# Performance work log

Hardware: AMD Instinct MI355X
Metric: run time of the kernel (lower is better)

## Reference

```python
import jax, jax.numpy as jnp
import numpy as np

DROPOUT_P = 0.5  # used as an additive constant in the normalizers, not as dropout
N = 384


def setup_inputs() -> dict:
    key = jax.random.key(0)
    k1, k2 = jax.random.split(key)
    inp = jax.random.uniform(k1, (N, N, N), dtype=jnp.float32)
    w = jax.random.uniform(k2, (N, N, N), dtype=jnp.float32)
    return {"input": inp, "w": w}


def reference(input, w):
    # e[i,j,l] = sum_k input[i,j,k] * w[l,k,j]
    e = jnp.einsum('ijk,lkj->ijl', input, w)
    # k (normalized by input row-sums) is dead code in the original forward;
    # only q and v feed the output, so we skip it.
    v = e  # second identical einsum in the source
    s_in = input.sum(axis=-1, keepdims=True)          # [N, N, 1]
    # einsum('ijk,ijl->ijl', input, w) == (sum_k input) * w
    q = s_in * w
    q = q / (DROPOUT_P + w.sum(axis=-1, keepdims=True))
    # causal mask: strict upper triangle set to -inf, broadcast over batch
    mask = jnp.triu(jnp.full((N, N), -jnp.inf, dtype=q.dtype), k=1)  # [N, N]
    attn = jax.nn.softmax(q + mask[None, :, :], axis=-1)              # [N, N, N]
    return jnp.matmul(attn, v)
```

## Files before the change

### kernel.cpp

```cpp
#include <hip/hip_runtime.h>
#include <hip/hip_bf16.h>


#define N 384
#define N2 (N * N)
#define BK 64
static const size_t N3 = (size_t)N * N * N;

typedef __attribute__((ext_vector_type(8))) short s16x8;
typedef __attribute__((ext_vector_type(4))) float f32x4;

#define AS1 __attribute__((address_space(1)))
#define AS3 __attribute__((address_space(3)))
__device__ __forceinline__ void gll16(const void* g, void* l) {
    __builtin_amdgcn_global_load_lds((const AS1 unsigned int*)g,
                                     (AS3 unsigned int*)l, 16, 0, 0);
}

__device__ __forceinline__ unsigned short f32_to_bf16(float f) {
    unsigned int u = __float_as_uint(f);
    u += 0x7FFFu + ((u >> 16) & 1u);
    return (unsigned short)(u >> 16);
}
__device__ __forceinline__ unsigned int pk2(float a, float b) {
    return (unsigned int)f32_to_bf16(a) | ((unsigned int)f32_to_bf16(b) << 16);
}

__global__ __launch_bounds__(256) void kT(const float* __restrict__ w,
                                          unsigned short* __restrict__ wt) {
    __shared__ unsigned short tile[64][68];
    const int r0 = blockIdx.x * 64;
    const int j0 = blockIdx.y * 64;
    const int tx = threadIdx.x & 63;
    const int ty = threadIdx.x >> 6;
#pragma unroll
    for (int p = 0; p < 16; ++p) {
        const int r = ty * 16 + p;
        tile[r][tx] = f32_to_bf16(w[(size_t)(r0 + r) * N + j0 + tx]);
    }
    __syncthreads();
#pragma unroll
    for (int p = 0; p < 16; ++p) {
        const int jj = ty * 16 + p;
        wt[(size_t)(j0 + jj) * N2 + r0 + tx] = tile[tx][jj];
    }
}

__global__ __launch_bounds__(256, 4) void k_e2(const float* __restrict__ in,
                                               const unsigned short* __restrict__ wt,
                                               unsigned short* __restrict__ e,
                                               float* __restrict__ rs) {
    __shared__ union {
        struct { unsigned short A[64 * 64]; unsigned short B[192 * 64]; } s;
        unsigned short C[64 * 200];
    } sm;

    const int lin = blockIdx.x;
    const int swz = (lin & 7) * 576 + (lin >> 3);
    const int j   = swz / 12;
    const int sub = swz % 12;
    const int i0  = (sub >> 1) * 64;
    const int l0  = (sub & 1) * 192;

    const int t = threadIdx.x, lane = t & 63, wv = t >> 6;
    const int fr = lane & 15, fx = lane >> 4;

    const int ra = t >> 2, ca = (t & 3) * 2;
    const float* Ab = in + (size_t)(i0 + ra) * N2 + (size_t)j * N + ca * 8;
    unsigned short* AsW0 = sm.s.A + ra * 64 + (((ca + 0) ^ (ra & 7)) * 8);
    unsigned short* AsW1 = sm.s.A + ra * 64 + (((ca + 1) ^ (ra & 7)) * 8);

    const unsigned short* Wj = wt + (size_t)j * N2 + (size_t)l0 * N;
    const int rb_off = lane >> 3;
    const int p8     = lane & 7;

    f32x4 acc[4][3];
#pragma unroll
    for (int m = 0; m < 4; ++m)
#pragma unroll
        for (int n = 0; n < 3; ++n) acc[m][n] = (f32x4){0.f, 0.f, 0.f, 0.f};

    float rsum = 0.f;

    float4 va[4];
    va[0] = *(const float4*)(Ab);
    va[1] = *(const float4*)(Ab + 4);
    va[2] = *(const float4*)(Ab + 8);
    va[3] = *(const float4*)(Ab + 12);

    for (int k0 = 0; k0 < N; k0 += BK) {
        __syncthreads();
        {
            rsum += (va[0].x + va[0].y + va[0].z + va[0].w) +
                    (va[1].x + va[1].y + va[1].z + va[1].w) +
                    (va[2].x + va[2].y + va[2].z + va[2].w) +
                    (va[3].x + va[3].y + va[3].z + va[3].w);
            uint4 a0, a1;
            a0.x = pk2(va[0].x, va[0].y); a0.y = pk2(va[0].z, va[0].w);
            a0.z = pk2(va[1].x, va[1].y); a0.w = pk2(va[1].z, va[1].w);
            a1.x = pk2(va[2].x, va[2].y); a1.y = pk2(va[2].z, va[2].w);
            a1.z = pk2(va[3].x, va[3].y); a1.w = pk2(va[3].z, va[3].w);
            *(uint4*)AsW0 = a0;
            *(uint4*)AsW1 = a1;
        }
#pragma unroll
        for (int itb = 0; itb < 6; ++itb) {
            const int rb = wv * 48 + itb * 8 + rb_off;
            const int sc = p8 ^ (rb & 7);
            gll16(Wj + (size_t)rb * N + k0 + sc * 8,
                  sm.s.B + (wv * 48 + itb * 8) * 64);
        }
        if (k0 + BK < N) {
            const float* An = Ab + k0 + BK;
            va[0] = *(const float4*)(An);
            va[1] = *(const float4*)(An + 4);
            va[2] = *(const float4*)(An + 8);
            va[3] = *(const float4*)(An + 12);
        }
        __syncthreads();
#pragma unroll
        for (int kk = 0; kk < 2; ++kk) {
            s16x8 af[4], bf[3];
#pragma unroll
            for (int m = 0; m < 4; ++m) {
                const int row = m * 16 + fr;
                const int x   = (kk * 4 + fx) ^ (row & 7);
                af[m] = *(const s16x8*)(sm.s.A + row * 64 + x * 8);
            }
#pragma unroll
            for (int n = 0; n < 3; ++n) {
                const int row = wv * 48 + n * 16 + fr;
                const int x   = (kk * 4 + fx) ^ (row & 7);
                bf[n] = *(const s16x8*)(sm.s.B + row * 64 + x * 8);
            }
#pragma unroll
            for (int m = 0; m < 4; ++m)
#pragma unroll
                for (int n = 0; n < 3; ++n)
                    acc[m][n] = __builtin_amdgcn_mfma_f32_16x16x32_bf16(
                        af[m], bf[n], acc[m][n], 0, 0, 0);
        }
    }

    rsum += __shfl_xor(rsum, 1, 64);
    rsum += __shfl_xor(rsum, 2, 64);
    if (rs != nullptr && l0 == 0 && (t & 3) == 0)
        rs[(size_t)(i0 + ra) * N + j] = rsum;

    __syncthreads();
#pragma unroll
    for (int m = 0; m < 4; ++m)
#pragma unroll
        for (int n = 0; n < 3; ++n)
#pragma unroll
            for (int r = 0; r < 4; ++r)
                sm.C[(m * 16 + fx * 4 + r) * 200 + wv * 48 + n * 16 + fr] =
                    f32_to_bf16(acc[m][n][r]);
    __syncthreads();
#pragma unroll
    for (int it = 0; it < 6; ++it) {
        const int cid = it * 256 + t;
        const int row = cid / 24;
        const int c   = cid % 24;
        *(uint4*)(e + (size_t)(i0 + row) * N2 + (size_t)j * N + l0 + c * 8) =
            *(const uint4*)&sm.C[row * 200 + c * 8];
    }
}

__global__ __launch_bounds__(256) void k_eT(const unsigned short* __restrict__ e,
                                            unsigned short* __restrict__ et) {
    __shared__ unsigned short tile[64][68];
    const int m0 = blockIdx.x * 64, l0 = blockIdx.y * 64;
    const size_t ib = (size_t)blockIdx.z * N2;
    const int t  = threadIdx.x;
    const int c4 = (t & 15) * 4, r = t >> 4;
#pragma unroll
    for (int p = 0; p < 4; ++p) {
        ushort4 v = *(const ushort4*)(e + ib + (size_t)(m0 + r + 16 * p) * N + l0 + c4);
        tile[c4 + 0][r + 16 * p] = v.x;
        tile[c4 + 1][r + 16 * p] = v.y;
        tile[c4 + 2][r + 16 * p] = v.z;
        tile[c4 + 3][r + 16 * p] = v.w;
    }
    __syncthreads();
#pragma unroll
    for (int p = 0; p < 4; ++p) {
        const int lr = r + 16 * p;
        ushort4 v = *(const ushort4*)&tile[lr][c4];
        *(ushort4*)(et + ib + (size_t)(l0 + lr) * N + m0 + c4) = v;
    }
}

template <bool HAVE_RS>
__global__ __launch_bounds__(256) void k_attn(const float* __restrict__ in,
                                              const float* __restrict__ w,
                                              const float* __restrict__ rs,
                                              unsigned short* __restrict__ attn) {
    const int row  = blockIdx.x * 4 + (threadIdx.x >> 6);
    const int lane = threadIdx.x & 63;
    const int jr   = row % N;

    const float2* wp = (const float2*)(w + (size_t)row * N);

    float2 wv[3];
    float rs_in = 0.f, rs_w = 0.f;
#pragma unroll
    for (int c = 0; c < 3; ++c) {
        wv[c] = wp[lane + 64 * c];
        rs_w += wv[c].x + wv[c].y;
    }
    if (HAVE_RS) {
#pragma unroll
        for (int s = 1; s < 64; s <<= 1) rs_w += __shfl_xor(rs_w, s, 64);
        rs_in = rs[row];
    } else {
        const float2* ip = (const float2*)(in + (size_t)row * N);
#pragma unroll
        for (int c = 0; c < 3; ++c) {
            float2 iv = ip[lane + 64 * c];
            rs_in += iv.x + iv.y;
        }
#pragma unroll
        for (int s = 1; s < 64; s <<= 1) {
            rs_in += __shfl_xor(rs_in, s, 64);
            rs_w  += __shfl_xor(rs_w, s, 64);
        }
    }
    const float scale = rs_in / (0.5f + rs_w);

    float2 q[3];
    float mx = -INFINITY;
#pragma unroll
    for (int c = 0; c < 3; ++c) {
        const int l = (lane + 64 * c) * 2;
        q[c].x = (l     <= jr) ? scale * wv[c].x : -INFINITY;
        q[c].y = (l + 1 <= jr) ? scale * wv[c].y : -INFINITY;
        mx = fmaxf(mx, fmaxf(q[c].x, q[c].y));
    }
#pragma unroll
    for (int s = 1; s < 64; s <<= 1) mx = fmaxf(mx, __shfl_xor(mx, s, 64));

    float2 p[3];
    float sum = 0.f;
#pragma unroll
    for (int c = 0; c < 3; ++c) {
        const int l = (lane + 64 * c) * 2;
        p[c].x = (l     <= jr) ? exp2f((q[c].x - mx) * 1.44269504f) : 0.f;
        p[c].y = (l + 1 <= jr) ? exp2f((q[c].y - mx) * 1.44269504f) : 0.f;
        sum += p[c].x + p[c].y;
    }
#pragma unroll
    for (int s = 1; s < 64; s <<= 1) sum += __shfl_xor(sum, s, 64);
    const float inv = 1.f / sum;
    unsigned int* ap = (unsigned int*)(attn + (size_t)row * N);
#pragma unroll
    for (int c = 0; c < 3; ++c)
        ap[lane + 64 * c] = pk2(p[c].x * inv, p[c].y * inv);
}

__global__ __launch_bounds__(256, 4) void k_av128(const unsigned short* __restrict__ attn,
                                                  const unsigned short* __restrict__ et,
                                                  float* __restrict__ out) {
    __shared__ union {
        struct { unsigned short A[128 * 64]; unsigned short B[128 * 64]; } s;
        float C[32 * 132];
    } sm;

    const int lin = blockIdx.x;
    const int swz = (lin & 7) * 432 + (lin >> 3);
    const int i   = swz / 9;
    const int sub = swz % 9;
    const int j0  = (sub / 3) * 128;
    const int l0  = (sub % 3) * 128;
    const int nt  = (j0 >> 6) + 2;

    const int t = threadIdx.x, lane = t & 63, wv = t >> 6;
    const int fr = lane & 15, fx = lane >> 4;
    const int wr = (wv >> 1) * 64;
    const int wc = (wv & 1) * 64;
    const int rb_off = lane >> 3;
    const int p8     = lane & 7;

    const unsigned short* Ag = attn + (size_t)i * N2 + (size_t)j0 * N;
    const unsigned short* Bg = et + (size_t)i * N2 + (size_t)l0 * N;

    f32x4 acc[4][4];
#pragma unroll
    for (int m = 0; m < 4; ++m)
#pragma unroll
        for (int n = 0; n < 4; ++n) acc[m][n] = (f32x4){0.f, 0.f, 0.f, 0.f};

    for (int tt = 0; tt < nt; ++tt) {
        const int k0 = tt * 64;
        __syncthreads();
#pragma unroll
        for (int op = 0; op < 4; ++op) {
            const int rr = wv * 32 + op * 8 + rb_off;
            const int sc = p8 ^ (rr & 7);
            gll16(Ag + (size_t)rr * N + k0 + sc * 8,
                  sm.s.A + (wv * 32 + op * 8) * 64);
        }
#pragma unroll
        for (int op = 0; op < 4; ++op) {
            const int rr = wv * 32 + op * 8 + rb_off;
            const int sc = p8 ^ (rr & 7);
            gll16(Bg + (size_t)rr * N + k0 + sc * 8,
                  sm.s.B + (wv * 32 + op * 8) * 64);
        }
        __syncthreads();
#pragma unroll
        for (int kk = 0; kk < 2; ++kk) {
            s16x8 af[4], bf[4];
#pragma unroll
            for (int m = 0; m < 4; ++m) {
                const int row = wr + m * 16 + fr;
                const int x   = (kk * 4 + fx) ^ (row & 7);
                af[m] = *(const s16x8*)(sm.s.A + row * 64 + x * 8);
            }
#pragma unroll
            for (int n = 0; n < 4; ++n) {
                const int row = wc + n * 16 + fr;
                const int x   = (kk * 4 + fx) ^ (row & 7);
                bf[n] = *(const s16x8*)(sm.s.B + row * 64 + x * 8);
            }
#pragma unroll
            for (int m = 0; m < 4; ++m)
#pragma unroll
                for (int n = 0; n < 4; ++n)
                    acc[m][n] = __builtin_amdgcn_mfma_f32_16x16x32_bf16(
                        af[m], bf[n], acc[m][n], 0, 0, 0);
        }
    }

    const int rq = fx * 4;
#pragma unroll
    for (int p = 0; p < 4; ++p) {
        __syncthreads();
        if ((wv >> 1) == (p >> 1)) {
            const int mbase = (p & 1) * 2;
#pragma unroll
            for (int mm = 0; mm < 2; ++mm)
#pragma unroll
                for (int n = 0; n < 4; ++n)
#pragma unroll
                    for (int r = 0; r < 4; ++r)
                        sm.C[(mm * 16 + rq + r) * 132 + wc + n * 16 + fr] =
                            acc[mbase + mm][n][r];
        }
        __syncthreads();
#pragma unroll
        for (int it = 0; it < 4; ++it) {
            const int cid = it * 256 + t;
            const int row = cid >> 5;
            const int c   = cid & 31;
            *(float4*)(out + (size_t)i * N2 + (size_t)(j0 + p * 32 + row) * N + l0 + c * 4) =
                *(const float4*)&sm.C[row * 132 + c * 4];
        }
    }
}

extern "C" void kernel_launch(void* const* d_in, const int* in_sizes, int n_in,
                              void* d_out, int out_size, void* d_ws, size_t ws_size,
                              hipStream_t stream) {
    const float* in = (const float*)d_in[0];
    const float* w  = (const float*)d_in[1];
    float* out      = (float*)d_out;

    unsigned short* r0 = (unsigned short*)d_ws;
    unsigned short* r1 = (unsigned short*)d_ws + N3;
    const bool have_rs = ws_size >= 2 * N3 * sizeof(unsigned short) + (size_t)N2 * sizeof(float);
    float* rs = have_rs ? (float*)((unsigned short*)d_ws + 2 * N3) : nullptr;

    kT<<<dim3(N2 / 64, N / 64), 256, 0, stream>>>(w, r0);
    k_e2<<<dim3(4608), 256, 0, stream>>>(in, r0, r1, rs);
    k_eT<<<dim3(6, 6, N), 256, 0, stream>>>(r1, r0);
    if (have_rs)
        k_attn<true><<<dim3(N2 / 4), 256, 0, stream>>>(in, w, rs, r1);
    else
        k_attn<false><<<dim3(N2 / 4), 256, 0, stream>>>(in, w, nullptr, r1);
    k_av128<<<dim3(3456), 256, 0, stream>>>(r1, r0, out);
}
```

Baseline: 394.0 us.

## Fuse e transpose into AV GEMM B-tile load, drop separate transpose kernel

Removes the standalone k_eT transpose pass. The AV GEMM now reads e directly with row-wise vector loads and transposes through registers into a padded, swizzled LDS B tile. This avoids a full N^3 bf16 read and write round trip plus one kernel launch. In exchange, the B operand no longer uses async global-to-LDS loads, LDS writes become scattered 8-byte stores, and the workspace grows to hold a separate attn buffer.

```diff
diff --git a/kernel.cpp b/kernel.cpp
--- a/kernel.cpp
+++ b/kernel.cpp
@@ -167,30 +167,6 @@
     }
 }
 
-__global__ __launch_bounds__(256) void k_eT(const unsigned short* __restrict__ e,
-                                            unsigned short* __restrict__ et) {
-    __shared__ unsigned short tile[64][68];
-    const int m0 = blockIdx.x * 64, l0 = blockIdx.y * 64;
-    const size_t ib = (size_t)blockIdx.z * N2;
-    const int t  = threadIdx.x;
-    const int c4 = (t & 15) * 4, r = t >> 4;
-#pragma unroll
-    for (int p = 0; p < 4; ++p) {
-        ushort4 v = *(const ushort4*)(e + ib + (size_t)(m0 + r + 16 * p) * N + l0 + c4);
-        tile[c4 + 0][r + 16 * p] = v.x;
-        tile[c4 + 1][r + 16 * p] = v.y;
-        tile[c4 + 2][r + 16 * p] = v.z;
-        tile[c4 + 3][r + 16 * p] = v.w;
-    }
-    __syncthreads();
-#pragma unroll
-    for (int p = 0; p < 4; ++p) {
-        const int lr = r + 16 * p;
-        ushort4 v = *(const ushort4*)&tile[lr][c4];
-        *(ushort4*)(et + ib + (size_t)(l0 + lr) * N + m0 + c4) = v;
-    }
-}
-
 template <bool HAVE_RS>
 __global__ __launch_bounds__(256) void k_attn(const float* __restrict__ in,
                                               const float* __restrict__ w,
@@ -258,11 +234,11 @@
         ap[lane + 64 * c] = pk2(p[c].x * inv, p[c].y * inv);
 }
 
-__global__ __launch_bounds__(256, 4) void k_av128(const unsigned short* __restrict__ attn,
-                                                  const unsigned short* __restrict__ et,
-                                                  float* __restrict__ out) {
+__global__ __launch_bounds__(256, 4) void k_av128t(const unsigned short* __restrict__ attn,
+                                                   const unsigned short* __restrict__ e,
+                                                   float* __restrict__ out) {
     __shared__ union {
-        struct { unsigned short A[128 * 64]; unsigned short B[128 * 64]; } s;
+        struct { unsigned short A[128 * 64]; unsigned short B[128 * 72]; } s;
         float C[32 * 132];
     } sm;
 
@@ -281,8 +257,13 @@
     const int rb_off = lane >> 3;
     const int p8     = lane & 7;
 
+    const int mg  = t & 15;
+    const int lcg = t >> 4;
+    const int bx  = (mg >> 1);
+    const int bh  = (mg & 1) * 4;
+
     const unsigned short* Ag = attn + (size_t)i * N2 + (size_t)j0 * N;
-    const unsigned short* Bg = et + (size_t)i * N2 + (size_t)l0 * N;
+    const unsigned short* Eg = e + (size_t)i * N2 + l0 + lcg * 8;
 
     f32x4 acc[4][4];
 #pragma unroll
@@ -300,12 +281,23 @@
             gll16(Ag + (size_t)rr * N + k0 + sc * 8,
                   sm.s.A + (wv * 32 + op * 8) * 64);
         }
-#pragma unroll
-        for (int op = 0; op < 4; ++op) {
-            const int rr = wv * 32 + op * 8 + rb_off;
-            const int sc = p8 ^ (rr & 7);
-            gll16(Bg + (size_t)rr * N + k0 + sc * 8,
-                  sm.s.B + (wv * 32 + op * 8) * 64);
+        {
+            uint4 bv0 = *(const uint4*)(Eg + (size_t)(k0 + mg * 4 + 0) * N);
+            uint4 bv1 = *(const uint4*)(Eg + (size_t)(k0 + mg * 4 + 1) * N);
+            uint4 bv2 = *(const uint4*)(Eg + (size_t)(k0 + mg * 4 + 2) * N);
+            uint4 bv3 = *(const uint4*)(Eg + (size_t)(k0 + mg * 4 + 3) * N);
+            const unsigned short* p0 = (const unsigned short*)&bv0;
+            const unsigned short* p1 = (const unsigned short*)&bv1;
+            const unsigned short* p2 = (const unsigned short*)&bv2;
+            const unsigned short* p3 = (const unsigned short*)&bv3;
+#pragma unroll
+            for (int q = 0; q < 8; ++q) {
+                const int l = lcg * 8 + q;
+                uint2 v;
+                v.x = (unsigned int)p0[q] | ((unsigned int)p1[q] << 16);
+                v.y = (unsigned int)p2[q] | ((unsigned int)p3[q] << 16);
+                *(uint2*)(sm.s.B + l * 72 + ((bx ^ (l & 7)) * 8) + bh) = v;
+            }
         }
         __syncthreads();
 #pragma unroll
@@ -321,7 +313,7 @@
             for (int n = 0; n < 4; ++n) {
                 const int row = wc + n * 16 + fr;
                 const int x   = (kk * 4 + fx) ^ (row & 7);
-                bf[n] = *(const s16x8*)(sm.s.B + row * 64 + x * 8);
+                bf[n] = *(const s16x8*)(sm.s.B + row * 72 + x * 8);
             }
 #pragma unroll
             for (int m = 0; m < 4; ++m)
@@ -366,17 +358,17 @@
     const float* w  = (const float*)d_in[1];
     float* out      = (float*)d_out;
 
-    unsigned short* r0 = (unsigned short*)d_ws;
-    unsigned short* r1 = (unsigned short*)d_ws + N3;
-    const bool have_rs = ws_size >= 2 * N3 * sizeof(unsigned short) + (size_t)N2 * sizeof(float);
-    float* rs = have_rs ? (float*)((unsigned short*)d_ws + 2 * N3) : nullptr;
+    unsigned short* r0   = (unsigned short*)d_ws;
+    unsigned short* r1   = (unsigned short*)d_ws + N3;
+    unsigned short* attn = (unsigned short*)d_ws + 2 * N3;
+    const bool have_rs = ws_size >= 3 * N3 * sizeof(unsigned short) + (size_t)N2 * sizeof(float);
+    float* rs = have_rs ? (float*)((unsigned short*)d_ws + 3 * N3) : nullptr;
 
     kT<<<dim3(N2 / 64, N / 64), 256, 0, stream>>>(w, r0);
     k_e2<<<dim3(4608), 256, 0, stream>>>(in, r0, r1, rs);
-    k_eT<<<dim3(6, 6, N), 256, 0, stream>>>(r1, r0);
     if (have_rs)
-        k_attn<true><<<dim3(N2 / 4), 256, 0, stream>>>(in, w, rs, r1);
+        k_attn<true><<<dim3(N2 / 4), 256, 0, stream>>>(in, w, rs, attn);
     else
-        k_attn<false><<<dim3(N2 / 4), 256, 0, stream>>>(in, w, nullptr, r1);
-    k_av128<<<dim3(3456), 256, 0, stream>>>(r1, r0, out);
-}
+        k_attn<false><<<dim3(N2 / 4), 256, 0, stream>>>(in, w, nullptr, attn);
+    k_av128t<<<dim3(3456), 256, 0, stream>>>(attn, r1, out);
+}
```

Result: slower. 413.8 us (+5.0%).

## Double-buffer B tiles and retile both batched GEMMs to 64x128 blocks

Applied to the files above, without the earlier changes.

Both the e-GEMM and the attn·V GEMM now double-buffer the B operand in LDS, prefetching the next k-slice with global_load_lds while MFMAs run on the current one. They use finer-grained waitcnt plus s_barrier and s_setprio in place of full __syncthreads. Tiles shrink to 64x128 per block with a 2x2 warp layout, doubling the grid. In the AV kernel the attn tile is loaded through registers, and the causal tile count now follows 64-row granularity, so less masked work is done. The aim is to hide load latency and improve load balance, at the cost of more blocks, re-reading B more often, and fragile hand-written wait counts.

```diff
diff --git a/kernel.cpp b/kernel.cpp
--- a/kernel.cpp
+++ b/kernel.cpp
@@ -16,6 +16,8 @@
     __builtin_amdgcn_global_load_lds((const AS1 unsigned int*)g,
                                      (AS3 unsigned int*)l, 16, 0, 0);
 }
+#define WAITL0 asm volatile("s_waitcnt lgkmcnt(0)" ::: "memory")
+#define BAR    __builtin_amdgcn_s_barrier()
 
 __device__ __forceinline__ unsigned short f32_to_bf16(float f) {
     unsigned int u = __float_as_uint(f);
@@ -46,24 +48,28 @@
     }
 }
 
-__global__ __launch_bounds__(256, 4) void k_e2(const float* __restrict__ in,
+__global__ __launch_bounds__(256, 4) void k_e3(const float* __restrict__ in,
                                                const unsigned short* __restrict__ wt,
                                                unsigned short* __restrict__ e,
                                                float* __restrict__ rs) {
     __shared__ union {
-        struct { unsigned short A[64 * 64]; unsigned short B[192 * 64]; } s;
-        unsigned short C[64 * 200];
+        struct { unsigned short A[64 * 64]; unsigned short B[2][128 * 64]; } s;
+        unsigned short C[64 * 136];
     } sm;
 
     const int lin = blockIdx.x;
-    const int swz = (lin & 7) * 576 + (lin >> 3);
-    const int j   = swz / 12;
-    const int sub = swz % 12;
-    const int i0  = (sub >> 1) * 64;
-    const int l0  = (sub & 1) * 192;
+    const int swz = (lin & 7) * 864 + (lin >> 3);
+    const int j   = swz / 18;
+    const int sub = swz % 18;
+    const int i0  = (sub / 3) * 64;
+    const int l0  = (sub % 3) * 128;
 
     const int t = threadIdx.x, lane = t & 63, wv = t >> 6;
     const int fr = lane & 15, fx = lane >> 4;
+    const int wr = (wv >> 1) * 32;
+    const int wc = (wv & 1) * 64;
+    const int rb_off = lane >> 3;
+    const int p8     = lane & 7;
 
     const int ra = t >> 2, ca = (t & 3) * 2;
     const float* Ab = in + (size_t)(i0 + ra) * N2 + (size_t)j * N + ca * 8;
@@ -71,14 +77,12 @@
     unsigned short* AsW1 = sm.s.A + ra * 64 + (((ca + 1) ^ (ra & 7)) * 8);
 
     const unsigned short* Wj = wt + (size_t)j * N2 + (size_t)l0 * N;
-    const int rb_off = lane >> 3;
-    const int p8     = lane & 7;
-
-    f32x4 acc[4][3];
-#pragma unroll
-    for (int m = 0; m < 4; ++m)
-#pragma unroll
-        for (int n = 0; n < 3; ++n) acc[m][n] = (f32x4){0.f, 0.f, 0.f, 0.f};
+
+    f32x4 acc[2][4];
+#pragma unroll
+    for (int m = 0; m < 2; ++m)
+#pragma unroll
+        for (int n = 0; n < 4; ++n) acc[m][n] = (f32x4){0.f, 0.f, 0.f, 0.f};
 
     float rsum = 0.f;
 
@@ -88,13 +92,27 @@
     va[2] = *(const float4*)(Ab + 8);
     va[3] = *(const float4*)(Ab + 12);
 
-    for (int k0 = 0; k0 < N; k0 += BK) {
-        __syncthreads();
+    {
+        unsigned short* B0 = sm.s.B[0];
+#pragma unroll
+        for (int op = 0; op < 4; ++op) {
+            const int rr = wv * 32 + op * 8 + rb_off;
+            const int sc = p8 ^ (rr & 7);
+            gll16(Wj + (size_t)rr * N + sc * 8, B0 + (wv * 32 + op * 8) * 64);
+        }
+        asm volatile("s_waitcnt vmcnt(0)" ::: "memory");
+    }
+
+    unsigned short* Bc = sm.s.B[0];
+    unsigned short* Bn = sm.s.B[1];
+
+#pragma unroll
+    for (int tt = 0; tt < 6; ++tt) {
+        rsum += (va[0].x + va[0].y + va[0].z + va[0].w) +
+                (va[1].x + va[1].y + va[1].z + va[1].w) +
+                (va[2].x + va[2].y + va[2].z + va[2].w) +
+                (va[3].x + va[3].y + va[3].z + va[3].w);
         {
-            rsum += (va[0].x + va[0].y + va[0].z + va[0].w) +
-                    (va[1].x + va[1].y + va[1].z + va[1].w) +
-                    (va[2].x + va[2].y + va[2].z + va[2].w) +
-                    (va[3].x + va[3].y + va[3].z + va[3].w);
             uint4 a0, a1;
             a0.x = pk2(va[0].x, va[0].y); a0.y = pk2(va[0].z, va[0].w);
             a0.z = pk2(va[1].x, va[1].y); a0.w = pk2(va[1].z, va[1].w);
@@ -103,43 +121,52 @@
             *(uint4*)AsW0 = a0;
             *(uint4*)AsW1 = a1;
         }
-#pragma unroll
-        for (int itb = 0; itb < 6; ++itb) {
-            const int rb = wv * 48 + itb * 8 + rb_off;
-            const int sc = p8 ^ (rb & 7);
-            gll16(Wj + (size_t)rb * N + k0 + sc * 8,
-                  sm.s.B + (wv * 48 + itb * 8) * 64);
-        }
-        if (k0 + BK < N) {
-            const float* An = Ab + k0 + BK;
+        if (tt < 5) {
+            const int kn = (tt + 1) * 64;
+#pragma unroll
+            for (int op = 0; op < 4; ++op) {
+                const int rr = wv * 32 + op * 8 + rb_off;
+                const int sc = p8 ^ (rr & 7);
+                gll16(Wj + (size_t)rr * N + kn + sc * 8, Bn + (wv * 32 + op * 8) * 64);
+            }
+            __builtin_amdgcn_sched_barrier(0);
+            const float* An = Ab + kn;
             va[0] = *(const float4*)(An);
             va[1] = *(const float4*)(An + 4);
             va[2] = *(const float4*)(An + 8);
             va[3] = *(const float4*)(An + 12);
         }
-        __syncthreads();
+        WAITL0;
+        BAR;
+        __builtin_amdgcn_s_setprio(1);
 #pragma unroll
         for (int kk = 0; kk < 2; ++kk) {
-            s16x8 af[4], bf[3];
-#pragma unroll
-            for (int m = 0; m < 4; ++m) {
-                const int row = m * 16 + fr;
+            s16x8 af[2], bf[4];
+#pragma unroll
+            for (int m = 0; m < 2; ++m) {
+                const int row = wr + m * 16 + fr;
                 const int x   = (kk * 4 + fx) ^ (row & 7);
                 af[m] = *(const s16x8*)(sm.s.A + row * 64 + x * 8);
             }
 #pragma unroll
-            for (int n = 0; n < 3; ++n) {
-                const int row = wv * 48 + n * 16 + fr;
+            for (int n = 0; n < 4; ++n) {
+                const int row = wc + n * 16 + fr;
                 const int x   = (kk * 4 + fx) ^ (row & 7);
-                bf[n] = *(const s16x8*)(sm.s.B + row * 64 + x * 8);
-            }
-#pragma unroll
-            for (int m = 0; m < 4; ++m)
-#pragma unroll
-                for (int n = 0; n < 3; ++n)
+                bf[n] = *(const s16x8*)(Bc + row * 64 + x * 8);
+            }
+#pragma unroll
+            for (int m = 0; m < 2; ++m)
+#pragma unroll
+                for (int n = 0; n < 4; ++n)
                     acc[m][n] = __builtin_amdgcn_mfma_f32_16x16x32_bf16(
                         af[m], bf[n], acc[m][n], 0, 0, 0);
         }
+        __builtin_amdgcn_s_setprio(0);
+        if (tt < 5) {
+            asm volatile("s_waitcnt vmcnt(4)" ::: "memory");
+        }
+        BAR;
+        unsigned short* tp = Bc; Bc = Bn; Bn = tp;
     }
 
     rsum += __shfl_xor(rsum, 1, 64);
@@ -148,22 +175,23 @@
         rs[(size_t)(i0 + ra) * N + j] = rsum;
 
     __syncthreads();
-#pragma unroll
-    for (int m = 0; m < 4; ++m)
-#pragma unroll
-        for (int n = 0; n < 3; ++n)
+    const int rq = fx * 4;
+#pragma unroll
+    for (int m = 0; m < 2; ++m)
+#pragma unroll
+        for (int n = 0; n < 4; ++n)
 #pragma unroll
             for (int r = 0; r < 4; ++r)
-                sm.C[(m * 16 + fx * 4 + r) * 200 + wv * 48 + n * 16 + fr] =
+                sm.C[(wr + m * 16 + rq + r) * 136 + wc + n * 16 + fr] =
                     f32_to_bf16(acc[m][n][r]);
     __syncthreads();
 #pragma unroll
-    for (int it = 0; it < 6; ++it) {
+    for (int it = 0; it < 4; ++it) {
         const int cid = it * 256 + t;
-        const int row = cid / 24;
-        const int c   = cid % 24;
+        const int row = cid >> 4;
+        const int c   = cid & 15;
         *(uint4*)(e + (size_t)(i0 + row) * N2 + (size_t)j * N + l0 + c * 8) =
-            *(const uint4*)&sm.C[row * 200 + c * 8];
+            *(const uint4*)&sm.C[row * 136 + c * 8];
     }
 }
 
@@ -258,61 +286,82 @@
         ap[lane + 64 * c] = pk2(p[c].x * inv, p[c].y * inv);
 }
 
-__global__ __launch_bounds__(256, 4) void k_av128(const unsigned short* __restrict__ attn,
-                                                  const unsigned short* __restrict__ et,
-                                                  float* __restrict__ out) {
+__global__ __launch_bounds__(256, 4) void k_av3(const unsigned short* __restrict__ attn,
+                                                const unsigned short* __restrict__ et,
+                                                float* __restrict__ out) {
     __shared__ union {
-        struct { unsigned short A[128 * 64]; unsigned short B[128 * 64]; } s;
-        float C[32 * 132];
+        struct { unsigned short A[64 * 64]; unsigned short B[2][128 * 64]; } s;
+        float C[64 * 132];
     } sm;
 
     const int lin = blockIdx.x;
-    const int swz = (lin & 7) * 432 + (lin >> 3);
-    const int i   = swz / 9;
-    const int sub = swz % 9;
-    const int j0  = (sub / 3) * 128;
+    const int swz = (lin & 7) * 864 + (lin >> 3);
+    const int i   = swz / 18;
+    const int sub = swz % 18;
+    const int j0  = (sub / 3) * 64;
     const int l0  = (sub % 3) * 128;
-    const int nt  = (j0 >> 6) + 2;
+    const int nt  = (j0 >> 6) + 1;
 
     const int t = threadIdx.x, lane = t & 63, wv = t >> 6;
     const int fr = lane & 15, fx = lane >> 4;
-    const int wr = (wv >> 1) * 64;
+    const int wr = (wv >> 1) * 32;
     const int wc = (wv & 1) * 64;
     const int rb_off = lane >> 3;
     const int p8     = lane & 7;
 
-    const unsigned short* Ag = attn + (size_t)i * N2 + (size_t)j0 * N;
+    const int ra = t >> 2, ca = (t & 3) * 2;
+    const unsigned short* Ab = attn + (size_t)i * N2 + (size_t)(j0 + ra) * N + ca * 8;
+    unsigned short* AsW0 = sm.s.A + ra * 64 + (((ca + 0) ^ (ra & 7)) * 8);
+    unsigned short* AsW1 = sm.s.A + ra * 64 + (((ca + 1) ^ (ra & 7)) * 8);
+
     const unsigned short* Bg = et + (size_t)i * N2 + (size_t)l0 * N;
 
-    f32x4 acc[4][4];
-#pragma unroll
-    for (int m = 0; m < 4; ++m)
+    f32x4 acc[2][4];
+#pragma unroll
+    for (int m = 0; m < 2; ++m)
 #pragma unroll
         for (int n = 0; n < 4; ++n) acc[m][n] = (f32x4){0.f, 0.f, 0.f, 0.f};
 
-    for (int tt = 0; tt < nt; ++tt) {
-        const int k0 = tt * 64;
-        __syncthreads();
+    uint4 va0 = *(const uint4*)(Ab);
+    uint4 va1 = *(const uint4*)(Ab + 8);
+
+    {
+        unsigned short* B0 = sm.s.B[0];
 #pragma unroll
         for (int op = 0; op < 4; ++op) {
             const int rr = wv * 32 + op * 8 + rb_off;
             const int sc = p8 ^ (rr & 7);
-            gll16(Ag + (size_t)rr * N + k0 + sc * 8,
-                  sm.s.A + (wv * 32 + op * 8) * 64);
-        }
-#pragma unroll
-        for (int op = 0; op < 4; ++op) {
-            const int rr = wv * 32 + op * 8 + rb_off;
-            const int sc = p8 ^ (rr & 7);
-            gll16(Bg + (size_t)rr * N + k0 + sc * 8,
-                  sm.s.B + (wv * 32 + op * 8) * 64);
-        }
-        __syncthreads();
+            gll16(Bg + (size_t)rr * N + sc * 8, B0 + (wv * 32 + op * 8) * 64);
+        }
+        asm volatile("s_waitcnt vmcnt(0)" ::: "memory");
+    }
+
+    unsigned short* Bc = sm.s.B[0];
+    unsigned short* Bn = sm.s.B[1];
+
+    for (int tt = 0; tt < nt; ++tt) {
+        *(uint4*)AsW0 = va0;
+        *(uint4*)AsW1 = va1;
+        if (tt + 1 < nt) {
+            const int kn = (tt + 1) * 64;
+#pragma unroll
+            for (int op = 0; op < 4; ++op) {
+                const int rr = wv * 32 + op * 8 + rb_off;
+                const int sc = p8 ^ (rr & 7);
+                gll16(Bg + (size_t)rr * N + kn + sc * 8, Bn + (wv * 32 + op * 8) * 64);
+            }
+            __builtin_amdgcn_sched_barrier(0);
+            va0 = *(const uint4*)(Ab + kn);
+            va1 = *(const uint4*)(Ab + kn + 8);
+        }
+        WAITL0;
+        BAR;
+        __builtin_amdgcn_s_setprio(1);
 #pragma unroll
         for (int kk = 0; kk < 2; ++kk) {
-            s16x8 af[4], bf[4];
-#pragma unroll
-            for (int m = 0; m < 4; ++m) {
+            s16x8 af[2], bf[4];
+#pragma unroll
+            for (int m = 0; m < 2; ++m) {
                 const int row = wr + m * 16 + fr;
                 const int x   = (kk * 4 + fx) ^ (row & 7);
                 af[m] = *(const s16x8*)(sm.s.A + row * 64 + x * 8);
@@ -321,41 +370,40 @@
             for (int n = 0; n < 4; ++n) {
                 const int row = wc + n * 16 + fr;
                 const int x   = (kk * 4 + fx) ^ (row & 7);
-                bf[n] = *(const s16x8*)(sm.s.B + row * 64 + x * 8);
-            }
-#pragma unroll
-            for (int m = 0; m < 4; ++m)
+                bf[n] = *(const s16x8*)(Bc + row * 64 + x * 8);
+            }
+#pragma unroll
+            for (int m = 0; m < 2; ++m)
 #pragma unroll
                 for (int n = 0; n < 4; ++n)
                     acc[m][n] = __builtin_amdgcn_mfma_f32_16x16x32_bf16(
                         af[m], bf[n], acc[m][n], 0, 0, 0);
         }
-    }
-
+        __builtin_amdgcn_s_setprio(0);
+        if (tt + 1 < nt) {
+            asm volatile("s_waitcnt vmcnt(2)" ::: "memory");
+        }
+        BAR;
+        unsigned short* tp = Bc; Bc = Bn; Bn = tp;
+    }
+
+    __syncthreads();
     const int rq = fx * 4;
 #pragma unroll
-    for (int p = 0; p < 4; ++p) {
-        __syncthreads();
-        if ((wv >> 1) == (p >> 1)) {
-            const int mbase = (p & 1) * 2;
-#pragma unroll
-            for (int mm = 0; mm < 2; ++mm)
-#pragma unroll
-                for (int n = 0; n < 4; ++n)
-#pragma unroll
-                    for (int r = 0; r < 4; ++r)
-                        sm.C[(mm * 16 + rq + r) * 132 + wc + n * 16 + fr] =
-                            acc[mbase + mm][n][r];
-        }
-        __syncthreads();
-#pragma unroll
-        for (int it = 0; it < 4; ++it) {
-            const int cid = it * 256 + t;
-            const int row = cid >> 5;
-            const int c   = cid & 31;
-            *(float4*)(out + (size_t)i * N2 + (size_t)(j0 + p * 32 + row) * N + l0 + c * 4) =
-                *(const float4*)&sm.C[row * 132 + c * 4];
-        }
+    for (int m = 0; m < 2; ++m)
+#pragma unroll
+        for (int n = 0; n < 4; ++n)
+#pragma unroll
+            for (int r = 0; r < 4; ++r)
+                sm.C[(wr + m * 16 + rq + r) * 132 + wc + n * 16 + fr] = acc[m][n][r];
+    __syncthreads();
+#pragma unroll
+    for (int it = 0; it < 8; ++it) {
+        const int cid = it * 256 + t;
+        const int row = cid >> 5;
+        const int c   = cid & 31;
+        *(float4*)(out + (size_t)i * N2 + (size_t)(j0 + row) * N + l0 + c * 4) =
+            *(const float4*)&sm.C[row * 132 + c * 4];
     }
 }
 
@@ -372,11 +420,11 @@
     float* rs = have_rs ? (float*)((unsigned short*)d_ws + 2 * N3) : nullptr;
 
     kT<<<dim3(N2 / 64, N / 64), 256, 0, stream>>>(w, r0);
-    k_e2<<<dim3(4608), 256, 0, stream>>>(in, r0, r1, rs);
+    k_e3<<<dim3(6912), 256, 0, stream>>>(in, r0, r1, rs);
     k_eT<<<dim3(6, 6, N), 256, 0, stream>>>(r1, r0);
     if (have_rs)
         k_attn<true><<<dim3(N2 / 4), 256, 0, stream>>>(in, w, rs, r1);
     else
         k_attn<false><<<dim3(N2 / 4), 256, 0, stream>>>(in, w, nullptr, r1);
-    k_av128<<<dim3(3456), 256, 0, stream>>>(r1, r0, out);
-}
+    k_av3<<<dim3(6912), 256, 0, stream>>>(r1, r0, out);
+}
```

After: 392.9 us, median of 2. About the same (-0.3%).
